# Kernel tuning notes

Measured on AMD Instinct MI355X. Metric: run time of the kernel, lower is better.

Reference implementation:

```python
import jax, jax.numpy as jnp
import numpy as np

N = 50000      # nodes
E = 800000     # edges (before self loops)
F_IN = 128     # input feature dim
H = 2          # attention heads
C = 64         # hidden channels per head (H*C = 128 = layer-2 input dim)
G = 64         # graphs in batch
OUT = 10       # out_channels
NEG_SLOPE = 0.2  # PyG GATConv default leaky relu slope


def setup_inputs() -> dict:
    key = jax.random.key(0)
    ks = jax.random.split(key, 16)
    sc = lambda f: np.float32(1.0 / np.sqrt(f))
    inp = {
        "x": jax.random.normal(ks[0], (N, F_IN), jnp.float32),
        "edge_index": jax.random.randint(ks[1], (2, E), 0, N, dtype=jnp.int32),
        "batch": jnp.sort(jax.random.randint(ks[2], (N,), 0, G, dtype=jnp.int32)),
        # GATConv layer 1 (lazy (-1,-1): separate src/dst projections)
        "Ws1": jax.random.normal(ks[3], (F_IN, H * C), jnp.float32) * sc(F_IN),
        "Wd1": jax.random.normal(ks[4], (F_IN, H * C), jnp.float32) * sc(F_IN),
        "as1": jax.random.normal(ks[5], (H, C), jnp.float32) * sc(C),
        "ad1": jax.random.normal(ks[6], (H, C), jnp.float32) * sc(C),
        "b1": jnp.zeros((H * C,), jnp.float32),
        # GATConv layer 2 (input dim = H*C = 128)
        "Ws2": jax.random.normal(ks[7], (H * C, H * C), jnp.float32) * sc(H * C),
        "Wd2": jax.random.normal(ks[8], (H * C, H * C), jnp.float32) * sc(H * C),
        "as2": jax.random.normal(ks[9], (H, C), jnp.float32) * sc(C),
        "ad2": jax.random.normal(ks[10], (H, C), jnp.float32) * sc(C),
        "b2": jnp.zeros((H * C,), jnp.float32),
        # final linear
        "Wl": jax.random.normal(ks[11], (H * C, OUT), jnp.float32) * sc(H * C),
        "bl": jnp.zeros((OUT,), jnp.float32),
    }
    return inp


def gat_conv(x, src, dst, Ws, Wd, att_s, att_d, b):
    # x: [N, F]; src/dst: [E'] (self loops already included)
    n = x.shape[0]
    xs = (x @ Ws).reshape(n, H, C)          # source-side projection
    xd = (x @ Wd).reshape(n, H, C)          # dest-side projection
    a_s = jnp.einsum('nhc,hc->nh', xs, att_s)   # [N, H]
    a_d = jnp.einsum('nhc,hc->nh', xd, att_d)   # [N, H]
    e = a_s[src] + a_d[dst]                      # [E', H]
    e = jnp.where(e > 0, e, NEG_SLOPE * e)       # leaky_relu
    # softmax over incoming edges per destination node (every node has a self loop)
    m = jax.ops.segment_max(e, dst, num_segments=n)
    ew = jnp.exp(e - m[dst])
    denom = jax.ops.segment_sum(ew, dst, num_segments=n)
    alpha = ew / denom[dst]                      # [E', H]
    out = jax.ops.segment_sum(alpha[:, :, None] * xs[src], dst, num_segments=n)
    return out.reshape(n, H * C) + b


def reference(x, edge_index, batch, Ws1, Wd1, as1, ad1, b1, Ws2, Wd2, as2, ad2, b2, Wl, bl):
    # add self loops once (add_self_loops=True)
    loops = jnp.arange(N, dtype=edge_index.dtype)
    src = jnp.concatenate([edge_index[0], loops])
    dst = jnp.concatenate([edge_index[1], loops])

    h = jax.nn.relu(gat_conv(x, src, dst, Ws1, Wd1, as1, ad1, b1))
    h = jax.nn.relu(gat_conv(h, src, dst, Ws2, Wd2, as2, ad2, b2))

    # global_mean_pool over batch vector
    sums = jax.ops.segment_sum(h, batch, num_segments=G)
    cnt = jax.ops.segment_sum(jnp.ones((N,), h.dtype), batch, num_segments=G)
    pooled = sums / jnp.maximum(cnt, 1.0)[:, None]

    # dropout(p=0.5) is identity in eval mode
    return pooled @ Wl + bl
```

## Files before the change

### kernel.cpp

```cpp
#include <hip/hip_runtime.h>
#include <hip/hip_bf16.h>

#define N_NODES 50000
#define N_EDGES 800000
#define N_GRAPHS 64
#define F_DIM 128
#define OUT_DIM 10
#define NB 391
#define EIDS_CAP 2560
#define SC_EDGES 4096
#define SC_BLOCKS ((N_EDGES + SC_EDGES - 1) / SC_EDGES)
#define POOL_CHUNK 128
#define POOL_BLOCKS ((N_NODES + POOL_CHUNK - 1) / POOL_CHUNK)

typedef __attribute__((ext_vector_type(8))) short short8;
typedef __attribute__((ext_vector_type(4))) float f32x4;

__device__ __forceinline__ unsigned int f2bf(float f) {
    unsigned int x; __builtin_memcpy(&x, &f, 4);
    return (x + 0x7fffu + ((x >> 16) & 1u)) >> 16;
}
__device__ __forceinline__ float bf2f(unsigned int u16) {
    unsigned int x = u16 << 16;
    float f; __builtin_memcpy(&f, &x, 4); return f;
}


__global__ __launch_bounds__(1024) void scatter_prep_kernel(
    const int* __restrict__ ei,
    const float* __restrict__ W1, const float* __restrict__ W2,
    const float* __restrict__ Wd1, const float* __restrict__ ad1,
    const float* __restrict__ Wd2, const float* __restrict__ ad2,
    unsigned short* __restrict__ Wt1, unsigned short* __restrict__ Wt2,
    float* __restrict__ weffd1, float* __restrict__ weffd2,
    uint4* __restrict__ zero_sums ,
    unsigned int* __restrict__ recs, int* __restrict__ exclT) {
    __shared__ unsigned int srec[SC_EDGES];
    __shared__ int hist[NB], lcur[NB];
    __shared__ int excl[512];
    int t = threadIdx.x;
    int blk = blockIdx.x;
    int tid = blk * 1024 + t;

    if (tid < 32768) {
        const float* W = (tid < 16384) ? W1 : W2;
        unsigned short* Wt = (tid < 16384) ? Wt1 : Wt2;
        int i = tid & 16383;
        int k = i >> 7, nn = i & 127;
        Wt[nn * 128 + k] = (unsigned short)f2bf(W[i]);
    } else if (tid < 33280) {
        int j = tid - 32768;
        const float* Wd = (j < 256) ? Wd1 : Wd2;
        const float* ad = (j < 256) ? ad1 : ad2;
        float* wout = (j < 256) ? weffd1 : weffd2;
        int i = j & 255, f = i >> 1, h = i & 1;
        const float4* wr = (const float4*)(Wd + f * 128 + h * 64);
        const float4* av = (const float4*)(ad + h * 64);
        float s = 0.f;
        #pragma unroll
        for (int c = 0; c < 16; ++c) {
            float4 w = wr[c], a = av[c];
            s += w.x*a.x + w.y*a.y + w.z*a.z + w.w*a.w;
        }
        wout[f * 2 + h] = s;
    } else if (tid < 35328) {
        zero_sums[tid - 33280] = make_uint4(0, 0, 0, 0);
    }

    int base = blk * SC_EDGES;
    for (int i = t; i < NB; i += 1024) { hist[i] = 0; lcur[i] = 0; }
    __syncthreads();
    unsigned int rec_[4]; int have[4];
    #pragma unroll
    for (int j = 0; j < 4; ++j) {
        int i = base + j * 1024 + t;
        have[j] = (i < N_EDGES);
        if (have[j]) {
            int src = ei[i], dst = ei[N_EDGES + i];
            int b = dst >> 7;
            rec_[j] = ((unsigned)b << 23) | ((unsigned)(dst & 127) << 16) | (unsigned)src;
            atomicAdd(&hist[b], 1);
        }
    }
    __syncthreads();
    if (t < 512) excl[t] = (t < NB) ? hist[t] : 0;
    __syncthreads();
    for (int off = 1; off < 512; off <<= 1) {
        int v = 0;
        if (t < 512 && t >= off) v = excl[t - off];
        __syncthreads();
        if (t < 512) excl[t] += v;
        __syncthreads();
    }
    #pragma unroll
    for (int j = 0; j < 4; ++j) {
        if (have[j]) {
            int b = rec_[j] >> 23;
            int pos = atomicAdd(&lcur[b], 1);
            srec[(excl[b] - hist[b]) + pos] = rec_[j];
        }
    }
    __syncthreads();
    int cnt = N_EDGES - base; if (cnt > SC_EDGES) cnt = SC_EDGES;
    for (int i = t; i < cnt; i += 1024)
        recs[(size_t)blk * SC_EDGES + i] = srec[i];
    if (t < NB) exclT[blk * NB + t] = excl[t];
}


__global__ __launch_bounds__(256) void gemm1_bucketize_kernel(
    const float* __restrict__ A, const unsigned short* __restrict__ Wt,
    const float* __restrict__ att_s, const float* __restrict__ weffd,
    const unsigned int* __restrict__ recs, const int* __restrict__ exclT,
    unsigned short* __restrict__ C, float* __restrict__ a_s, float* __restrict__ a_d,
    unsigned short* __restrict__ eids, int2* __restrict__ rsre, int n) {
    __shared__ unsigned int srec[EIDS_CAP];
    __shared__ int lo0[SC_BLOCKS], cntb[SC_BLOCKS];
    __shared__ int sc[256];
    __shared__ int pexcl[SC_BLOCKS + 1];
    __shared__ int hist[128], excl[128], cur[128];
    int t = threadIdx.x;

    if (blockIdx.x < NB) {
        int b = blockIdx.x;
        int nvalid = n - b * 128; if (nvalid > 128) nvalid = 128;
        if (t < 128) { hist[t] = 0; cur[t] = 0; }
        for (int i = t; i < SC_BLOCKS; i += 256) {
            int hi = exclT[i * NB + b];
            int l  = b ? exclT[i * NB + b - 1] : 0;
            lo0[i] = l; cntb[i] = hi - l;
        }
        __syncthreads();
        sc[t] = (t < SC_BLOCKS) ? cntb[t] : 0;
        __syncthreads();
        for (int off = 1; off < 256; off <<= 1) {
            int v = (t >= off) ? sc[t - off] : 0;
            __syncthreads();
            sc[t] += v;
            __syncthreads();
        }
        if (t < SC_BLOCKS) pexcl[t] = sc[t] - cntb[t];
        if (t == 0) pexcl[SC_BLOCKS] = sc[255];
        __syncthreads();
        int total = pexcl[SC_BLOCKS];
        int maxsc = EIDS_CAP - 128;
        if (total > maxsc) total = maxsc;
        for (int i = t; i < total; i += 256) {
            int l = 0, h = SC_BLOCKS;
            while (l + 1 < h) { int m = (l + h) >> 1; if (pexcl[m] <= i) l = m; else h = m; }
            unsigned int rec = recs[(size_t)l * SC_EDGES + lo0[l] + (i - pexcl[l])];
            srec[i] = rec;
            atomicAdd(&hist[(rec >> 16) & 127], 1);
        }
        __syncthreads();
        if (t < nvalid) hist[t] += 1;
        __syncthreads();
        if (t < 128) excl[t] = hist[t];
        __syncthreads();
        for (int off = 1; off < 128; off <<= 1) {
            int v = 0;
            if (t < 128 && t >= off) v = excl[t - off];
            __syncthreads();
            if (t < 128) excl[t] += v;
            __syncthreads();
        }
        int base2 = b * EIDS_CAP;
        if (t < nvalid) {
            int st = excl[t] - hist[t];
            rsre[b * 128 + t] = make_int2(base2 + st, base2 + excl[t]);
            eids[base2 + st] = (unsigned short)(b * 128 + t);
            cur[t] = 1;
        }
        __syncthreads();
        for (int i = t; i < total; i += 256) {
            unsigned int rec = srec[i];
            int dl = (rec >> 16) & 127;
            int pos = atomicAdd(&cur[dl], 1);
            eids[base2 + (excl[dl] - hist[dl]) + pos] = (unsigned short)(rec & 0xffffu);
        }
    }

    int l = t & 63;
    int quad = l >> 4, lr = l & 15;
    int m0 = blockIdx.x * 64 + (t >> 6) * 16;
    int arow = m0 + lr; if (arow >= n) arow = n - 1;

    short8 afrag[4];
    float pd0 = 0.f, pd1 = 0.f;
    const float2* wd2 = (const float2*)weffd;
    #pragma unroll
    for (int kb = 0; kb < 4; ++kb) {
        const float4* ap = (const float4*)(A + (size_t)arow * 128 + kb * 32 + quad * 8);
        float4 a0 = ap[0], a1 = ap[1];
        int k0 = kb * 32 + quad * 8;
        float2 w0 = wd2[k0+0], w1 = wd2[k0+1], w2 = wd2[k0+2], w3 = wd2[k0+3];
        float2 w4 = wd2[k0+4], w5 = wd2[k0+5], w6 = wd2[k0+6], w7 = wd2[k0+7];
        pd0 += a0.x*w0.x + a0.y*w1.x + a0.z*w2.x + a0.w*w3.x
             + a1.x*w4.x + a1.y*w5.x + a1.z*w6.x + a1.w*w7.x;
        pd1 += a0.x*w0.y + a0.y*w1.y + a0.z*w2.y + a0.w*w3.y
             + a1.x*w4.y + a1.y*w5.y + a1.z*w6.y + a1.w*w7.y;
        short8 s;
        s[0] = (short)f2bf(a0.x); s[1] = (short)f2bf(a0.y);
        s[2] = (short)f2bf(a0.z); s[3] = (short)f2bf(a0.w);
        s[4] = (short)f2bf(a1.x); s[5] = (short)f2bf(a1.y);
        s[6] = (short)f2bf(a1.z); s[7] = (short)f2bf(a1.w);
        afrag[kb] = s;
    }
    pd0 += __shfl_xor(pd0, 16); pd0 += __shfl_xor(pd0, 32);
    pd1 += __shfl_xor(pd1, 16); pd1 += __shfl_xor(pd1, 32);
    if (l < 16 && m0 + lr < n) *(float2*)(a_d + (size_t)(m0 + lr) * 2) = make_float2(pd0, pd1);

    f32x4 acc[8] = {};
    #pragma unroll
    for (int nt = 0; nt < 8; ++nt) {
        #pragma unroll
        for (int kb = 0; kb < 4; ++kb) {
            short8 b = *(const short8*)(Wt + (size_t)(nt * 16 + lr) * 128 + kb * 32 + quad * 8);
            acc[nt] = __builtin_amdgcn_mfma_f32_16x16x32_bf16(afrag[kb], b, acc[nt], 0, 0, 0);
        }
    }
    float asv[8];
    #pragma unroll
    for (int nt = 0; nt < 8; ++nt) asv[nt] = att_s[nt * 16 + lr];
    float pa0[4] = {}, pa1[4] = {};
    #pragma unroll
    for (int nt = 0; nt < 8; ++nt)
        #pragma unroll
        for (int r = 0; r < 4; ++r) {
            if (nt < 4) pa0[r] += acc[nt][r] * asv[nt];
            else        pa1[r] += acc[nt][r] * asv[nt];
        }
    #pragma unroll
    for (int d = 1; d < 16; d <<= 1) {
        #pragma unroll
        for (int r = 0; r < 4; ++r) {
            pa0[r] += __shfl_xor(pa0[r], d);
            pa1[r] += __shfl_xor(pa1[r], d);
        }
    }
    if (lr == 0) {
        #pragma unroll
        for (int r = 0; r < 4; ++r) {
            int row = m0 + quad * 4 + r;
            if (row < n) *(float2*)(a_s + (size_t)row * 2) = make_float2(pa0[r], pa1[r]);
        }
    }
    #pragma unroll
    for (int nt = 0; nt < 8; ++nt)
        #pragma unroll
        for (int r = 0; r < 4; ++r) {
            int row = m0 + quad * 4 + r;
            if (row < n)
                C[(size_t)row * 128 + nt * 16 + lr] = (unsigned short)f2bf(acc[nt][r]);
        }
}


__global__ __launch_bounds__(256) void gemm_fused_bf16_kernel(
    const unsigned short* __restrict__ A, const unsigned short* __restrict__ Wt,
    const float* __restrict__ att_s, const float* __restrict__ weffd,
    unsigned short* __restrict__ C, float* __restrict__ a_s, float* __restrict__ a_d, int n) {
    int t = threadIdx.x;
    int l = t & 63;
    int quad = l >> 4, lr = l & 15;
    int m0 = blockIdx.x * 64 + (t >> 6) * 16;
    int arow = m0 + lr; if (arow >= n) arow = n - 1;

    short8 afrag[4];
    float pd0 = 0.f, pd1 = 0.f;
    const float2* wd2 = (const float2*)weffd;
    #pragma unroll
    for (int kb = 0; kb < 4; ++kb) {
        short8 s = *(const short8*)(A + (size_t)arow * 128 + kb * 32 + quad * 8);
        afrag[kb] = s;
        const unsigned int* u = (const unsigned int*)&s;
        int k0 = kb * 32 + quad * 8;
        #pragma unroll
        for (int d = 0; d < 4; ++d) {
            float x0 = __uint_as_float(u[d] << 16);
            float x1 = __uint_as_float(u[d] & 0xffff0000u);
            float2 wv0 = wd2[k0 + 2*d], wv1 = wd2[k0 + 2*d + 1];
            pd0 += x0 * wv0.x + x1 * wv1.x;
            pd1 += x0 * wv0.y + x1 * wv1.y;
        }
    }
    pd0 += __shfl_xor(pd0, 16); pd0 += __shfl_xor(pd0, 32);
    pd1 += __shfl_xor(pd1, 16); pd1 += __shfl_xor(pd1, 32);
    if (l < 16 && m0 + lr < n) *(float2*)(a_d + (size_t)(m0 + lr) * 2) = make_float2(pd0, pd1);

    f32x4 acc[8] = {};
    #pragma unroll
    for (int nt = 0; nt < 8; ++nt) {
        #pragma unroll
        for (int kb = 0; kb < 4; ++kb) {
            short8 b = *(const short8*)(Wt + (size_t)(nt * 16 + lr) * 128 + kb * 32 + quad * 8);
            acc[nt] = __builtin_amdgcn_mfma_f32_16x16x32_bf16(afrag[kb], b, acc[nt], 0, 0, 0);
        }
    }
    float asv[8];
    #pragma unroll
    for (int nt = 0; nt < 8; ++nt) asv[nt] = att_s[nt * 16 + lr];
    float pa0[4] = {}, pa1[4] = {};
    #pragma unroll
    for (int nt = 0; nt < 8; ++nt)
        #pragma unroll
        for (int r = 0; r < 4; ++r) {
            if (nt < 4) pa0[r] += acc[nt][r] * asv[nt];
            else        pa1[r] += acc[nt][r] * asv[nt];
        }
    #pragma unroll
    for (int d = 1; d < 16; d <<= 1) {
        #pragma unroll
        for (int r = 0; r < 4; ++r) {
            pa0[r] += __shfl_xor(pa0[r], d);
            pa1[r] += __shfl_xor(pa1[r], d);
        }
    }
    if (lr == 0) {
        #pragma unroll
        for (int r = 0; r < 4; ++r) {
            int row = m0 + quad * 4 + r;
            if (row < n) *(float2*)(a_s + (size_t)row * 2) = make_float2(pa0[r], pa1[r]);
        }
    }
    #pragma unroll
    for (int nt = 0; nt < 8; ++nt)
        #pragma unroll
        for (int r = 0; r < 4; ++r) {
            int row = m0 + quad * 4 + r;
            if (row < n)
                C[(size_t)row * 128 + nt * 16 + lr] = (unsigned short)f2bf(acc[nt][r]);
        }
}


#define AGG_GRP(EIV, PME, X0, X1, Y0, Y1, JB)                                   \
    {                                                                           \
        _Pragma("unroll")                                                       \
        for (int u = 0; u < 4; ++u) {                                           \
            int j = (JB) + u;                                                   \
            int srcn = __shfl((EIV), j);                                        \
            float pj = __shfl((PME), j + hoff);                                 \
            unsigned int v = xs32[(size_t)srcn * 64 + lane];                    \
            float v0 = __uint_as_float(v << 16);                                \
            float v1 = __uint_as_float(v & 0xffff0000u);                        \
            if (u & 1) { Y0 += pj * v0; Y1 += pj * v1; }                        \
            else       { X0 += pj * v0; X1 += pj * v1; }                        \
        }                                                                       \
    }

__global__ __launch_bounds__(256) void aggregate_kernel(
    const int2* __restrict__ rsre, const unsigned short* __restrict__ eids,
    const float* __restrict__ a_s, const float* __restrict__ a_d,
    const unsigned int* __restrict__ xs32, const float* __restrict__ bias,
    unsigned int* __restrict__ out32, int npairs) {
    int wv = (int)((blockIdx.x * blockDim.x + threadIdx.x) >> 6);
    int lane = threadIdx.x & 63;
    if (wv >= npairs) return;
    int d0 = wv * 2, d1 = d0 + 1;
    int h = lane >> 5, j32 = lane & 31, hoff = h << 5, ch = lane * 2;
    float2 adp0 = *(const float2*)(a_d + (size_t)d0 * 2);
    float2 adp1 = *(const float2*)(a_d + (size_t)d1 * 2);
    float adv0 = (h == 0) ? adp0.x : adp0.y;
    float adv1 = (h == 0) ? adp1.x : adp1.y;
    int2 r0 = rsre[d0], r1 = rsre[d1];
    int b0 = r0.x, e0 = r0.y, b1 = r1.x, e1 = r1.y;

    float xA0 = 0, xA1 = 0, yA0 = 0, yA1 = 0;
    float xB0 = 0, xB1 = 0, yB0 = 0, yB1 = 0;
    float ls0 = 0, ls1 = 0;
    while (b0 < e0 || b1 < e1) {
        int k0 = e0 - b0; k0 = k0 < 0 ? 0 : (k0 > 32 ? 32 : k0);
        int k1 = e1 - b1; k1 = k1 < 0 ? 0 : (k1 > 32 ? 32 : k1);
        int ei0 = 0, ei1 = 0;
        float pm0 = 0.f, pm1 = 0.f;
        if (k0 > 0) {
            ei0 = (int)eids[b0 + (j32 < k0 ? j32 : k0 - 1)];
            float2 as2 = *(const float2*)(a_s + (size_t)ei0 * 2);
            float ev = ((h == 0) ? as2.x : as2.y) + adv0;
            ev = (ev > 0.f) ? ev : 0.2f * ev;
            pm0 = (j32 < k0) ? __expf(ev) : 0.f;
            ls0 += pm0;
        }
        if (k1 > 0) {
            ei1 = (int)eids[b1 + (j32 < k1 ? j32 : k1 - 1)];
            float2 as2 = *(const float2*)(a_s + (size_t)ei1 * 2);
            float ev = ((h == 0) ? as2.x : as2.y) + adv1;
            ev = (ev > 0.f) ? ev : 0.2f * ev;
            pm1 = (j32 < k1) ? __expf(ev) : 0.f;
            ls1 += pm1;
        }
        int jb0 = 0, jb1 = 0;
        while (jb0 + 4 <= k0 && jb1 + 4 <= k1) {
            AGG_GRP(ei0, pm0, xA0, xA1, yA0, yA1, jb0)
            AGG_GRP(ei1, pm1, xB0, xB1, yB0, yB1, jb1)
            jb0 += 4; jb1 += 4;
        }
        for (; jb0 + 4 <= k0; jb0 += 4) AGG_GRP(ei0, pm0, xA0, xA1, yA0, yA1, jb0)
        for (; jb1 + 4 <= k1; jb1 += 4) AGG_GRP(ei1, pm1, xB0, xB1, yB0, yB1, jb1)
        for (; jb0 < k0; ++jb0) {
            int srcn = __shfl(ei0, jb0);
            float pj = __shfl(pm0, jb0 + hoff);
            unsigned int v = xs32[(size_t)srcn * 64 + lane];
            xA0 += pj * __uint_as_float(v << 16);
            xA1 += pj * __uint_as_float(v & 0xffff0000u);
        }
        for (; jb1 < k1; ++jb1) {
            int srcn = __shfl(ei1, jb1);
            float pj = __shfl(pm1, jb1 + hoff);
            unsigned int v = xs32[(size_t)srcn * 64 + lane];
            xB0 += pj * __uint_as_float(v << 16);
            xB1 += pj * __uint_as_float(v & 0xffff0000u);
        }
        b0 += k0; b1 += k1;
    }
    #pragma unroll
    for (int d = 1; d <= 16; d <<= 1) {
        ls0 += __shfl_xor(ls0, d);
        ls1 += __shfl_xor(ls1, d);
    }
    float inv0 = 1.f / ls0, inv1 = 1.f / ls1;
    float bc0 = bias[ch], bc1 = bias[ch + 1];
    float o00 = fmaxf((xA0 + yA0) * inv0 + bc0, 0.f);
    float o01 = fmaxf((xA1 + yA1) * inv0 + bc1, 0.f);
    float o10 = fmaxf((xB0 + yB0) * inv1 + bc0, 0.f);
    float o11 = fmaxf((xB1 + yB1) * inv1 + bc1, 0.f);
    out32[(size_t)d0 * 64 + lane] = f2bf(o00) | (f2bf(o01) << 16);
    out32[(size_t)d1 * 64 + lane] = f2bf(o10) | (f2bf(o11) << 16);
}


__global__ __launch_bounds__(256) void pool_partial_kernel(
    const unsigned short* __restrict__ Hf, const int* __restrict__ batch,
    float* __restrict__ sums, int n) {
    int t = threadIdx.x;
    int c = t & 127, half = t >> 7;
    int start = blockIdx.x * POOL_CHUNK;
    int end = min(start + POOL_CHUNK, n);
    float acc = 0.f;
    int cur = -1;
    for (int i = start + half; i < end; i += 2) {
        int g = batch[i];
        if (g != cur) {
            if (cur >= 0) atomicAdd(&sums[cur * 128 + c], acc);
            acc = 0.f; cur = g;
        }
        acc += bf2f(Hf[(size_t)i * 128 + c]);
    }
    if (cur >= 0) atomicAdd(&sums[cur * 128 + c], acc);
}

__global__ void final_linear_kernel(const float* __restrict__ sums,
                                    const int* __restrict__ batch,
                                    const float* __restrict__ Wl, const float* __restrict__ bl,
                                    float* __restrict__ out, int n) {
    int t = blockIdx.x * blockDim.x + threadIdx.x;
    if (t >= N_GRAPHS * OUT_DIM) return;
    int g = t / OUT_DIM, o = t % OUT_DIM;
    int lo = 0, hi = n;
    while (lo < hi) { int mid = (lo + hi) >> 1; if (batch[mid] < g) lo = mid + 1; else hi = mid; }
    int s0 = lo; hi = n;
    while (lo < hi) { int mid = (lo + hi) >> 1; if (batch[mid] < g + 1) lo = mid + 1; else hi = mid; }
    float cnt = (float)(lo - s0);
    float inv = 1.f / fmaxf(cnt, 1.f);
    float s = bl[o];
    for (int c = 0; c < 128; ++c) s += sums[g * 128 + c] * inv * Wl[c * OUT_DIM + o];
    out[g * OUT_DIM + o] = s;
}


extern "C" void kernel_launch(void* const* d_in, const int* in_sizes, int n_in,
                              void* d_out, int out_size, void* d_ws, size_t ws_size,
                              hipStream_t stream) {
    const float* x    = (const float*)d_in[0];
    const int*   ei   = (const int*)d_in[1];
    const int*   batch= (const int*)d_in[2];
    const float* Ws1  = (const float*)d_in[3];
    const float* Wd1  = (const float*)d_in[4];
    const float* as1  = (const float*)d_in[5];
    const float* ad1  = (const float*)d_in[6];
    const float* b1   = (const float*)d_in[7];
    const float* Ws2  = (const float*)d_in[8];
    const float* Wd2  = (const float*)d_in[9];
    const float* as2  = (const float*)d_in[10];
    const float* ad2  = (const float*)d_in[11];
    const float* b2   = (const float*)d_in[12];
    const float* Wl   = (const float*)d_in[13];
    const float* bl   = (const float*)d_in[14];
    float* out = (float*)d_out;

    char* p = (char*)d_ws;
    auto alloc = [&](size_t bytes) {
        void* r = (void*)p;
        p += (bytes + 255) & ~(size_t)255;
        return r;
    };
    int* exclT    = (int*)alloc(sizeof(int) * SC_BLOCKS * NB);
    unsigned int* recs = (unsigned int*)alloc(sizeof(int) * (size_t)SC_BLOCKS * SC_EDGES);
    unsigned short* eids = (unsigned short*)alloc(sizeof(short) * (size_t)NB * EIDS_CAP);
    int2* rsre    = (int2*)alloc(sizeof(int2) * N_NODES);
    float* a_s    = (float*)alloc(sizeof(float) * N_NODES * 2);
    float* a_d    = (float*)alloc(sizeof(float) * N_NODES * 2);
    float* sums   = (float*)alloc(sizeof(float) * N_GRAPHS * 128);
    float* weffd1 = (float*)alloc(sizeof(float) * 128 * 2);
    float* weffd2 = (float*)alloc(sizeof(float) * 128 * 2);
    unsigned short* Wt1  = (unsigned short*)alloc(sizeof(short) * 128 * 128);
    unsigned short* Wt2  = (unsigned short*)alloc(sizeof(short) * 128 * 128);
    unsigned short* bufA = (unsigned short*)alloc(sizeof(short) * (size_t)N_NODES * F_DIM);
    unsigned short* bufB = (unsigned short*)alloc(sizeof(short) * (size_t)N_NODES * F_DIM);

    const int gemm_grid = (N_NODES + 63) / 64;
    const int npairs    = N_NODES / 2;
    const int agg_grid  = (npairs + 3) / 4;

    scatter_prep_kernel<<<SC_BLOCKS, 1024, 0, stream>>>(ei, Ws1, Ws2, Wd1, ad1, Wd2, ad2,
                                                        Wt1, Wt2, weffd1, weffd2,
                                                        (uint4*)sums, recs, exclT);

    gemm1_bucketize_kernel<<<gemm_grid, 256, 0, stream>>>(x, Wt1, as1, weffd1,
                                                          recs, exclT,
                                                          bufA, a_s, a_d,
                                                          eids, rsre, N_NODES);
    aggregate_kernel<<<agg_grid, 256, 0, stream>>>(rsre, eids, a_s, a_d,
                                                   (const unsigned int*)bufA, b1,
                                                   (unsigned int*)bufB, npairs);

    gemm_fused_bf16_kernel<<<gemm_grid, 256, 0, stream>>>(bufB, Wt2, as2, weffd2,
                                                          bufA, a_s, a_d, N_NODES);
    aggregate_kernel<<<agg_grid, 256, 0, stream>>>(rsre, eids, a_s, a_d,
                                                   (const unsigned int*)bufA, b2,
                                                   (unsigned int*)bufB, npairs);

    pool_partial_kernel<<<POOL_BLOCKS, 256, 0, stream>>>(bufB, batch, sums, N_NODES);
    final_linear_kernel<<<(N_GRAPHS * OUT_DIM + 255) / 256, 256, 0, stream>>>(sums, batch, Wl, bl, out, N_NODES);
}
```

Measured before the change: 265.5 us.

## Bucketize edges into 64-node buckets across all GEMM blocks and localize pooling

The edge bucketing now uses 64-node destination buckets with 2048-edge scatter blocks, so all 782 GEMM blocks each build one bucket instead of only the first 391 doing bucket work. This spreads the CSR construction evenly across the grid and removes the imbalance where half the blocks carried extra work. The pooling kernel also gains vectorized bf16 loads and shared-memory accumulation for the first two graphs in each chunk, which cuts global atomics. In exchange, the per-bucket capacity is tighter (EIDS_HALF=1408) and the scatter prefix scan widens to 1024 entries.

```diff
diff --git a/kernel.cpp b/kernel.cpp
--- a/kernel.cpp
+++ b/kernel.cpp
@@ -6,10 +6,10 @@
 #define N_GRAPHS 64
 #define F_DIM 128
 #define OUT_DIM 10
-#define NB 391
-#define EIDS_CAP 2560
-#define SC_EDGES 4096
-#define SC_BLOCKS ((N_EDGES + SC_EDGES - 1) / SC_EDGES)
+#define NB2 782
+#define NREG 392
+#define SC_EDGES 2048
+#define EIDS_HALF 1408
 #define POOL_CHUNK 128
 #define POOL_BLOCKS ((N_NODES + POOL_CHUNK - 1) / POOL_CHUNK)
 
@@ -36,8 +36,8 @@
     uint4* __restrict__ zero_sums ,
     unsigned int* __restrict__ recs, int* __restrict__ exclT) {
     __shared__ unsigned int srec[SC_EDGES];
-    __shared__ int hist[NB], lcur[NB];
-    __shared__ int excl[512];
+    __shared__ int hist[NB2], lcur[NB2];
+    __shared__ int excl[1024];
     int t = threadIdx.x;
     int blk = blockIdx.x;
     int tid = blk * 1024 + t;
@@ -68,43 +68,42 @@
     }
 
     int base = blk * SC_EDGES;
-    for (int i = t; i < NB; i += 1024) { hist[i] = 0; lcur[i] = 0; }
+    for (int i = t; i < NB2; i += 1024) { hist[i] = 0; lcur[i] = 0; }
     __syncthreads();
-    unsigned int rec_[4]; int have[4];
-    #pragma unroll
-    for (int j = 0; j < 4; ++j) {
+    unsigned int rec_[2]; int have[2];
+    #pragma unroll
+    for (int j = 0; j < 2; ++j) {
         int i = base + j * 1024 + t;
         have[j] = (i < N_EDGES);
         if (have[j]) {
             int src = ei[i], dst = ei[N_EDGES + i];
-            int b = dst >> 7;
-            rec_[j] = ((unsigned)b << 23) | ((unsigned)(dst & 127) << 16) | (unsigned)src;
-            atomicAdd(&hist[b], 1);
+            int b2 = dst >> 6;
+            rec_[j] = ((unsigned)b2 << 22) | ((unsigned)(dst & 63) << 16) | (unsigned)src;
+            atomicAdd(&hist[b2], 1);
         }
     }
     __syncthreads();
-    if (t < 512) excl[t] = (t < NB) ? hist[t] : 0;
+    excl[t] = (t < NB2) ? hist[t] : 0;
     __syncthreads();
-    for (int off = 1; off < 512; off <<= 1) {
-        int v = 0;
-        if (t < 512 && t >= off) v = excl[t - off];
-        __syncthreads();
-        if (t < 512) excl[t] += v;
-        __syncthreads();
-    }
-    #pragma unroll
-    for (int j = 0; j < 4; ++j) {
+    for (int off = 1; off < 1024; off <<= 1) {
+        int v = (t >= off) ? excl[t - off] : 0;
+        __syncthreads();
+        excl[t] += v;
+        __syncthreads();
+    }
+    #pragma unroll
+    for (int j = 0; j < 2; ++j) {
         if (have[j]) {
-            int b = rec_[j] >> 23;
-            int pos = atomicAdd(&lcur[b], 1);
-            srec[(excl[b] - hist[b]) + pos] = rec_[j];
+            int b2 = rec_[j] >> 22;
+            int pos = atomicAdd(&lcur[b2], 1);
+            srec[(excl[b2] - hist[b2]) + pos] = rec_[j];
         }
     }
     __syncthreads();
     int cnt = N_EDGES - base; if (cnt > SC_EDGES) cnt = SC_EDGES;
     for (int i = t; i < cnt; i += 1024)
         recs[(size_t)blk * SC_EDGES + i] = srec[i];
-    if (t < NB) exclT[blk * NB + t] = excl[t];
+    if (t < NB2) exclT[blk * NB2 + t] = excl[t];
 }
 
 
@@ -114,24 +113,26 @@
     const unsigned int* __restrict__ recs, const int* __restrict__ exclT,
     unsigned short* __restrict__ C, float* __restrict__ a_s, float* __restrict__ a_d,
     unsigned short* __restrict__ eids, int2* __restrict__ rsre, int n) {
-    __shared__ unsigned int srec[EIDS_CAP];
-    __shared__ int lo0[SC_BLOCKS], cntb[SC_BLOCKS];
+    __shared__ unsigned int srec[EIDS_HALF];
+    __shared__ int lo0[NREG], cntb[NREG];
     __shared__ int sc[256];
-    __shared__ int pexcl[SC_BLOCKS + 1];
-    __shared__ int hist[128], excl[128], cur[128];
+    __shared__ int pexcl[NREG + 1];
+    __shared__ int hist[64], excl[64], cur[64];
     int t = threadIdx.x;
-
-    if (blockIdx.x < NB) {
-        int b = blockIdx.x;
-        int nvalid = n - b * 128; if (nvalid > 128) nvalid = 128;
-        if (t < 128) { hist[t] = 0; cur[t] = 0; }
-        for (int i = t; i < SC_BLOCKS; i += 256) {
-            int hi = exclT[i * NB + b];
-            int l  = b ? exclT[i * NB + b - 1] : 0;
-            lo0[i] = l; cntb[i] = hi - l;
-        }
-        __syncthreads();
-        sc[t] = (t < SC_BLOCKS) ? cntb[t] : 0;
+    int b2 = blockIdx.x;
+
+    {
+        int nvalid = n - b2 * 64; if (nvalid > 64) nvalid = 64; if (nvalid < 0) nvalid = 0;
+        if (t < 64) { hist[t] = 0; cur[t] = 0; }
+        for (int r = t; r < NREG; r += 256) {
+            int hi = exclT[r * NB2 + b2];
+            int l  = b2 ? exclT[r * NB2 + b2 - 1] : 0;
+            lo0[r] = l; cntb[r] = hi - l;
+        }
+        __syncthreads();
+        int c0 = (2 * t < NREG) ? cntb[2 * t] : 0;
+        int c1 = (2 * t + 1 < NREG) ? cntb[2 * t + 1] : 0;
+        sc[t] = c0 + c1;
         __syncthreads();
         for (int off = 1; off < 256; off <<= 1) {
             int v = (t >= off) ? sc[t - off] : 0;
@@ -139,42 +140,44 @@
             sc[t] += v;
             __syncthreads();
         }
-        if (t < SC_BLOCKS) pexcl[t] = sc[t] - cntb[t];
-        if (t == 0) pexcl[SC_BLOCKS] = sc[255];
-        __syncthreads();
-        int total = pexcl[SC_BLOCKS];
-        int maxsc = EIDS_CAP - 128;
+        int ex = sc[t] - (c0 + c1);
+        if (2 * t < NREG) pexcl[2 * t] = ex;
+        if (2 * t + 1 < NREG) pexcl[2 * t + 1] = ex + c0;
+        if (t == 255) pexcl[NREG] = sc[255];
+        __syncthreads();
+        int total = pexcl[NREG];
+        int maxsc = EIDS_HALF - 64;
         if (total > maxsc) total = maxsc;
         for (int i = t; i < total; i += 256) {
-            int l = 0, h = SC_BLOCKS;
+            int l = 0, h = NREG;
             while (l + 1 < h) { int m = (l + h) >> 1; if (pexcl[m] <= i) l = m; else h = m; }
             unsigned int rec = recs[(size_t)l * SC_EDGES + lo0[l] + (i - pexcl[l])];
             srec[i] = rec;
-            atomicAdd(&hist[(rec >> 16) & 127], 1);
+            atomicAdd(&hist[(rec >> 16) & 63], 1);
         }
         __syncthreads();
         if (t < nvalid) hist[t] += 1;
         __syncthreads();
-        if (t < 128) excl[t] = hist[t];
-        __syncthreads();
-        for (int off = 1; off < 128; off <<= 1) {
+        if (t < 64) excl[t] = hist[t];
+        __syncthreads();
+        for (int off = 1; off < 64; off <<= 1) {
             int v = 0;
-            if (t < 128 && t >= off) v = excl[t - off];
+            if (t < 64 && t >= off) v = excl[t - off];
             __syncthreads();
-            if (t < 128) excl[t] += v;
+            if (t < 64) excl[t] += v;
             __syncthreads();
         }
-        int base2 = b * EIDS_CAP;
+        int base2 = b2 * EIDS_HALF;
         if (t < nvalid) {
             int st = excl[t] - hist[t];
-            rsre[b * 128 + t] = make_int2(base2 + st, base2 + excl[t]);
-            eids[base2 + st] = (unsigned short)(b * 128 + t);
+            rsre[b2 * 64 + t] = make_int2(base2 + st, base2 + excl[t]);
+            eids[base2 + st] = (unsigned short)(b2 * 64 + t);
             cur[t] = 1;
         }
         __syncthreads();
         for (int i = t; i < total; i += 256) {
             unsigned int rec = srec[i];
-            int dl = (rec >> 16) & 127;
+            int dl = (rec >> 16) & 63;
             int pos = atomicAdd(&cur[dl], 1);
             eids[base2 + (excl[dl] - hist[dl]) + pos] = (unsigned short)(rec & 0xffffu);
         }
@@ -433,21 +436,53 @@
 __global__ __launch_bounds__(256) void pool_partial_kernel(
     const unsigned short* __restrict__ Hf, const int* __restrict__ batch,
     float* __restrict__ sums, int n) {
+    __shared__ float acc2[2][128];
+    __shared__ int sgf;
     int t = threadIdx.x;
-    int c = t & 127, half = t >> 7;
+    acc2[t >> 7][t & 127] = 0.f;
     int start = blockIdx.x * POOL_CHUNK;
     int end = min(start + POOL_CHUNK, n);
-    float acc = 0.f;
+    if (t == 0) sgf = batch[start];
+    __syncthreads();
+    int gfirst = sgf;
+    int c4 = (t & 31) * 4;
+    int sub = t >> 5;
+    float a0 = 0, a1 = 0, a2 = 0, a3 = 0;
     int cur = -1;
-    for (int i = start + half; i < end; i += 2) {
+    for (int i = start + sub; i < end; i += 8) {
         int g = batch[i];
         if (g != cur) {
-            if (cur >= 0) atomicAdd(&sums[cur * 128 + c], acc);
-            acc = 0.f; cur = g;
-        }
-        acc += bf2f(Hf[(size_t)i * 128 + c]);
-    }
-    if (cur >= 0) atomicAdd(&sums[cur * 128 + c], acc);
+            if (cur >= 0) {
+                int idx = cur - gfirst;
+                if (idx < 2) {
+                    atomicAdd(&acc2[idx][c4+0], a0); atomicAdd(&acc2[idx][c4+1], a1);
+                    atomicAdd(&acc2[idx][c4+2], a2); atomicAdd(&acc2[idx][c4+3], a3);
+                } else {
+                    atomicAdd(&sums[cur*128+c4+0], a0); atomicAdd(&sums[cur*128+c4+1], a1);
+                    atomicAdd(&sums[cur*128+c4+2], a2); atomicAdd(&sums[cur*128+c4+3], a3);
+                }
+                a0 = a1 = a2 = a3 = 0.f;
+            }
+            cur = g;
+        }
+        uint2 v = *(const uint2*)(Hf + (size_t)i * 128 + c4);
+        a0 += bf2f(v.x & 0xffffu); a1 += bf2f(v.x >> 16);
+        a2 += bf2f(v.y & 0xffffu); a3 += bf2f(v.y >> 16);
+    }
+    if (cur >= 0) {
+        int idx = cur - gfirst;
+        if (idx < 2) {
+            atomicAdd(&acc2[idx][c4+0], a0); atomicAdd(&acc2[idx][c4+1], a1);
+            atomicAdd(&acc2[idx][c4+2], a2); atomicAdd(&acc2[idx][c4+3], a3);
+        } else {
+            atomicAdd(&sums[cur*128+c4+0], a0); atomicAdd(&sums[cur*128+c4+1], a1);
+            atomicAdd(&sums[cur*128+c4+2], a2); atomicAdd(&sums[cur*128+c4+3], a3);
+        }
+    }
+    __syncthreads();
+    int g = gfirst + (t >> 7);
+    float v = acc2[t >> 7][t & 127];
+    if (g < N_GRAPHS && v != 0.f) atomicAdd(&sums[g * 128 + (t & 127)], v);
 }
 
 __global__ void final_linear_kernel(const float* __restrict__ sums,
@@ -495,9 +530,9 @@
         p += (bytes + 255) & ~(size_t)255;
         return r;
     };
-    int* exclT    = (int*)alloc(sizeof(int) * SC_BLOCKS * NB);
-    unsigned int* recs = (unsigned int*)alloc(sizeof(int) * (size_t)SC_BLOCKS * SC_EDGES);
-    unsigned short* eids = (unsigned short*)alloc(sizeof(short) * (size_t)NB * EIDS_CAP);
+    int* exclT    = (int*)alloc(sizeof(int) * NREG * NB2);
+    unsigned int* recs = (unsigned int*)alloc(sizeof(int) * (size_t)NREG * SC_EDGES);
+    unsigned short* eids = (unsigned short*)alloc(sizeof(short) * (size_t)NB2 * EIDS_HALF);
     int2* rsre    = (int2*)alloc(sizeof(int2) * N_NODES);
     float* a_s    = (float*)alloc(sizeof(float) * N_NODES * 2);
     float* a_d    = (float*)alloc(sizeof(float) * N_NODES * 2);
@@ -513,9 +548,9 @@
     const int npairs    = N_NODES / 2;
     const int agg_grid  = (npairs + 3) / 4;
 
-    scatter_prep_kernel<<<SC_BLOCKS, 1024, 0, stream>>>(ei, Ws1, Ws2, Wd1, ad1, Wd2, ad2,
-                                                        Wt1, Wt2, weffd1, weffd2,
-                                                        (uint4*)sums, recs, exclT);
+    scatter_prep_kernel<<<NREG, 1024, 0, stream>>>(ei, Ws1, Ws2, Wd1, ad1, Wd2, ad2,
+                                                   Wt1, Wt2, weffd1, weffd2,
+                                                   (uint4*)sums, recs, exclT);
 
     gemm1_bucketize_kernel<<<gemm_grid, 256, 0, stream>>>(x, Wt1, as1, weffd1,
                                                           recs, exclT,
```

Result: no change. 265.5 us (-0.0%).
